# Performance work log

Measured on AMD Instinct MI355X. Metric: run time of the kernel, lower is better.

Reference implementation:

```python
import jax, jax.numpy as jnp
import numpy as np

IN_FEATURES = 4096
OUT_FEATURES = 4096
TOKENS = 8192
DENSITY = 0.5


def setup_inputs() -> dict:
    key = jax.random.key(0)
    kx, kw, km, kb = jax.random.split(key, 4)
    X = jax.random.normal(kx, (TOKENS, IN_FEATURES), dtype=jnp.float32)
    # kaiming-uniform-like init for weight [out, in]
    bound_w = np.sqrt(6.0 / IN_FEATURES) / np.sqrt(1.0 + 5.0)
    W = jax.random.uniform(kw, (OUT_FEATURES, IN_FEATURES), dtype=jnp.float32,
                           minval=-bound_w, maxval=bound_w)
    mask = jax.random.bernoulli(km, DENSITY, (OUT_FEATURES, IN_FEATURES))
    bound_b = 1.0 / np.sqrt(IN_FEATURES)
    b = jax.random.uniform(kb, (OUT_FEATURES,), dtype=jnp.float32,
                           minval=-bound_b, maxval=bound_b)
    return {"X": X, "W": W, "mask": mask, "b": b}


def reference(X, W, mask, b):
    # F.linear with a fixed-mask sparse weight: y = X @ (W * mask)^T + b
    Wm = W * mask.astype(W.dtype)  # masked weight [out, in]
    return jnp.einsum('ti,oi->to', X, Wm) + b
```

## Files before the change

### kernel.cpp

```cpp
#include <hip/hip_runtime.h>
#include <hip/hip_bf16.h>
#include <cstdint>
#include <cstddef>

#define M_TOK 8192
#define K_IN  4096
#define N_OUT 4096
#define NKS   384

typedef __attribute__((ext_vector_type(8))) short short8;
typedef __attribute__((ext_vector_type(4))) unsigned short ushort4v;
typedef __attribute__((ext_vector_type(4))) float f32x4;

__device__ inline void split_bf16(float x, unsigned short& h, unsigned short& l) {
    unsigned int u = __float_as_uint(x);
    unsigned int hb = (u + 0x7FFFu + ((u >> 16) & 1u)) >> 16;
    h = (unsigned short)hb;
    float hf = __uint_as_float(hb << 16);
    float r = x - hf;
    unsigned int ur = __float_as_uint(r);
    unsigned int lb = (ur + 0x7FFFu + ((ur >> 16) & 1u)) >> 16;
    l = (unsigned short)lb;
}

__global__ __launch_bounds__(256) void sl_cvt_x(const float* __restrict__ X,
                                                unsigned short* __restrict__ hi,
                                                unsigned short* __restrict__ lo, int n4) {
    int stride = gridDim.x * blockDim.x;
    for (int g = blockIdx.x * blockDim.x + threadIdx.x; g < n4; g += stride) {
        float4 v = ((const float4*)X)[g];
        float f[4] = {v.x, v.y, v.z, v.w};
        ushort4v h, l;
#pragma unroll
        for (int i = 0; i < 4; ++i) {
            unsigned short hh, ll;
            split_bf16(f[i], hh, ll);
            h[i] = hh; l[i] = ll;
        }
        ((ushort4v*)hi)[g] = h;
        ((ushort4v*)lo)[g] = l;
    }
}

__global__ __launch_bounds__(256) void sl_cvt_w(const float* __restrict__ W,
                                                const int* __restrict__ mask,
                                                unsigned short* __restrict__ hi,
                                                unsigned short* __restrict__ lo, int n4) {
    int stride = gridDim.x * blockDim.x;
    for (int g = blockIdx.x * blockDim.x + threadIdx.x; g < n4; g += stride) {
        float4 v = ((const float4*)W)[g];
        int4  mm = ((const int4*)mask)[g];
        float f[4];
        f[0] = mm.x ? v.x : 0.f;  f[1] = mm.y ? v.y : 0.f;
        f[2] = mm.z ? v.z : 0.f;  f[3] = mm.w ? v.w : 0.f;
        ushort4v h, l;
#pragma unroll
        for (int i = 0; i < 4; ++i) {
            unsigned short hh, ll;
            split_bf16(f[i], hh, ll);
            h[i] = hh; l[i] = ll;
        }
        ((ushort4v*)hi)[g] = h;
        ((ushort4v*)lo)[g] = l;
    }
}

__device__ inline void gload16(const void* g, void* l) {
    __builtin_amdgcn_global_load_lds(
        (const __attribute__((address_space(1))) void*)g,
        (__attribute__((address_space(3))) void*)l, 16, 0, 0);
}

__global__ __launch_bounds__(512, 2)
void sl_gemm_bf16x3(const unsigned short* __restrict__ Xhi,
                    const unsigned short* __restrict__ Xlo,
                    const unsigned short* __restrict__ Whi,
                    const unsigned short* __restrict__ Wlo,
                    const float* __restrict__ bias,
                    float* __restrict__ out) {
    __shared__ __align__(16) unsigned short As[4][256][32];
    __shared__ __align__(16) unsigned short Bs[4][256][32];

    const int bid = blockIdx.x;
    const int swz = (bid & 7) * 64 + (bid >> 3);
    const int bm = swz >> 4;
    const int bn = swz & 15;
    const int brow = bm * 256;
    const int bcol = bn * 256;

    const int tid = threadIdx.x;
    const int w   = tid >> 6;
    const int wm  = w >> 2, wn = w & 3;
    const int l   = tid & 63;
    const int r   = l & 15;
    const int kg  = l >> 4;

    const int swzCol = (((tid & 3) ^ ((tid >> 3) & 3)) * 8);
    const size_t aRow0 = (size_t)(brow + (tid >> 2)) * K_IN + swzCol;
    const size_t aRow1 = aRow0 + (size_t)128 * K_IN;
    const size_t bRow0 = (size_t)(bcol + (tid >> 2)) * K_IN + swzCol;
    const size_t bRow1 = bRow0 + (size_t)128 * K_IN;

    char* AsB = (char*)&As[0][0][0];
    char* BsB = (char*)&Bs[0][0][0];
    const int woff = w * 1024;

    const unsigned short* AsE = &As[0][0][0];
    const unsigned short* BsE = &Bs[0][0][0];
    const int slotOff = (kg ^ ((r >> 1) & 3)) * 8;
    const int aBaseE = (wm * 128 + r) * 32 + slotOff;
    const int bBaseE = (wn * 64 + r) * 32 + slotOff;

    f32x4 acc[8][4];
#pragma unroll
    for (int m = 0; m < 8; ++m)
#pragma unroll
        for (int n = 0; n < 4; ++n)
            acc[m][n] = (f32x4){0.f, 0.f, 0.f, 0.f};

#define STAGE_A(s_) do {                                                   \
    const int seg_ = (s_) >> 7;                                            \
    const unsigned short* pA_ = (seg_ == 1) ? Xlo : Xhi;                   \
    const size_t k_ = (size_t)((s_) & 127) * 32;                           \
    char* d_ = AsB + ((s_) & 3) * 16384 + woff;                            \
    gload16(pA_ + aRow0 + k_, d_);                                         \
    gload16(pA_ + aRow1 + k_, d_ + 8192);                                  \
} while (0)

#define STAGE_B(s_) do {                                                   \
    const int seg_ = (s_) >> 7;                                            \
    const unsigned short* pB_ = (seg_ == 2) ? Wlo : Whi;                   \
    const size_t k_ = (size_t)((s_) & 127) * 32;                           \
    char* d_ = BsB + ((s_) & 3) * 16384 + woff;                            \
    gload16(pB_ + bRow0 + k_, d_);                                         \
    gload16(pB_ + bRow1 + k_, d_ + 8192);                                  \
} while (0)

    STAGE_A(0); STAGE_B(0);
    STAGE_A(1); STAGE_B(1);
    STAGE_A(2); STAGE_B(2);

    for (int s = 0; s < NKS; ++s) {
        asm volatile("s_waitcnt vmcnt(8)" ::: "memory");
        __builtin_amdgcn_s_barrier();
        __builtin_amdgcn_sched_barrier(0);

        const int buf = (s & 3) * 8192;
        const bool st = (s + 3) < NKS;
        if (st) STAGE_A(s + 3);

        short8 a[4], b[4];
#pragma unroll
        for (int n = 0; n < 4; ++n)
            b[n] = *(const short8*)(BsE + buf + bBaseE + n * 512);
#pragma unroll
        for (int m = 0; m < 4; ++m)
            a[m] = *(const short8*)(AsE + buf + aBaseE + m * 512);

        __builtin_amdgcn_s_setprio(1);
#pragma unroll
        for (int m = 0; m < 4; ++m)
#pragma unroll
            for (int n = 0; n < 4; ++n)
                acc[m][n] = __builtin_amdgcn_mfma_f32_16x16x32_bf16(a[m], b[n], acc[m][n], 0, 0, 0);
        __builtin_amdgcn_s_setprio(0);

        if (st) STAGE_B(s + 3);
#pragma unroll
        for (int m = 0; m < 4; ++m)
            a[m] = *(const short8*)(AsE + buf + aBaseE + (m + 4) * 512);

        __builtin_amdgcn_s_setprio(1);
#pragma unroll
        for (int m = 0; m < 4; ++m)
#pragma unroll
            for (int n = 0; n < 4; ++n)
                acc[m + 4][n] = __builtin_amdgcn_mfma_f32_16x16x32_bf16(a[m], b[n], acc[m + 4][n], 0, 0, 0);
        __builtin_amdgcn_s_setprio(0);
    }
#undef STAGE_A
#undef STAGE_B

    float bv[4];
#pragma unroll
    for (int n = 0; n < 4; ++n)
        bv[n] = bias[bcol + wn * 64 + n * 16 + r];
    const int colBase = bcol + wn * 64 + r;
#pragma unroll
    for (int m = 0; m < 8; ++m) {
        const size_t rowb = (size_t)(brow + wm * 128 + m * 16 + kg * 4);
#pragma unroll
        for (int n = 0; n < 4; ++n) {
            const size_t c = (size_t)(colBase + n * 16);
#pragma unroll
            for (int q = 0; q < 4; ++q)
                out[(rowb + q) * N_OUT + c] = acc[m][n][q] + bv[n];
        }
    }
}

__global__ void sl_naive(const float* __restrict__ X, const float* __restrict__ W,
                         const int* __restrict__ mask, const float* __restrict__ bias,
                         float* __restrict__ out) {
    int o = blockIdx.x * blockDim.x + threadIdx.x;
    int t = blockIdx.y;
    if (o >= N_OUT) return;
    const float* xr = X + (size_t)t * K_IN;
    const float* wr = W + (size_t)o * K_IN;
    const int*   mr = mask + (size_t)o * K_IN;
    float s = 0.f;
    for (int k = 0; k < K_IN; ++k)
        s += xr[k] * (mr[k] ? wr[k] : 0.f);
    out[(size_t)t * N_OUT + o] = s + bias[o];
}

extern "C" void kernel_launch(void* const* d_in, const int* in_sizes, int n_in,
                              void* d_out, int out_size, void* d_ws, size_t ws_size,
                              hipStream_t stream) {
    (void)in_sizes; (void)n_in; (void)out_size;
    const float* X    = (const float*)d_in[0];
    const float* W    = (const float*)d_in[1];
    const int*   mask = (const int*)d_in[2];
    const float* bias = (const float*)d_in[3];
    float* out = (float*)d_out;

    const size_t xplane = (size_t)M_TOK * K_IN;
    const size_t wplane = (size_t)N_OUT * K_IN;
    const size_t need = (2 * xplane + 2 * wplane) * sizeof(unsigned short);

    if (ws_size < need) {
        dim3 g((N_OUT + 255) / 256, M_TOK);
        sl_naive<<<g, 256, 0, stream>>>(X, W, mask, bias, out);
        return;
    }

    unsigned short* Xhi = (unsigned short*)d_ws;
    unsigned short* Xlo = Xhi + xplane;
    unsigned short* Whi = Xlo + xplane;
    unsigned short* Wlo = Whi + wplane;

    sl_cvt_x<<<2048, 256, 0, stream>>>(X, Xhi, Xlo, (int)(xplane / 4));
    sl_cvt_w<<<2048, 256, 0, stream>>>(W, mask, Whi, Wlo, (int)(wplane / 4));
    sl_gemm_bf16x3<<<512, 512, 0, stream>>>(Xhi, Xlo, Whi, Wlo, bias, out);
}
```

Baseline: 1.139 ms.

## Fuse X/W conversion kernels and restructure GEMM loop into barrier-synced ping-pong phases

Merges the two bf16 hi/lo split kernels into a single launch that handles X and W on separate block ranges, with 8 elements per thread. In the GEMM main loop, the LDS fragment loads for each half are issued before the global-to-LDS prefetch, and the waits now sit inside each iteration at four block-wide barriers around the two MFMA clusters. The aim is to save one launch and to interleave memory and MFMA phases across waves. The extra barriers per k-step can add synchronization stalls if waves fail to overlap as intended.

```diff
diff --git a/kernel.cpp b/kernel.cpp
--- a/kernel.cpp
+++ b/kernel.cpp
@@ -9,7 +9,7 @@
 #define NKS   384
 
 typedef __attribute__((ext_vector_type(8))) short short8;
-typedef __attribute__((ext_vector_type(4))) unsigned short ushort4v;
+typedef __attribute__((ext_vector_type(8))) unsigned short ushort8;
 typedef __attribute__((ext_vector_type(4))) float f32x4;
 
 __device__ inline void split_bf16(float x, unsigned short& h, unsigned short& l) {
@@ -23,45 +23,54 @@
     l = (unsigned short)lb;
 }
 
-__global__ __launch_bounds__(256) void sl_cvt_x(const float* __restrict__ X,
-                                                unsigned short* __restrict__ hi,
-                                                unsigned short* __restrict__ lo, int n4) {
-    int stride = gridDim.x * blockDim.x;
-    for (int g = blockIdx.x * blockDim.x + threadIdx.x; g < n4; g += stride) {
-        float4 v = ((const float4*)X)[g];
-        float f[4] = {v.x, v.y, v.z, v.w};
-        ushort4v h, l;
-#pragma unroll
-        for (int i = 0; i < 4; ++i) {
-            unsigned short hh, ll;
-            split_bf16(f[i], hh, ll);
-            h[i] = hh; l[i] = ll;
-        }
-        ((ushort4v*)hi)[g] = h;
-        ((ushort4v*)lo)[g] = l;
-    }
-}
-
-__global__ __launch_bounds__(256) void sl_cvt_w(const float* __restrict__ W,
-                                                const int* __restrict__ mask,
-                                                unsigned short* __restrict__ hi,
-                                                unsigned short* __restrict__ lo, int n4) {
-    int stride = gridDim.x * blockDim.x;
-    for (int g = blockIdx.x * blockDim.x + threadIdx.x; g < n4; g += stride) {
-        float4 v = ((const float4*)W)[g];
-        int4  mm = ((const int4*)mask)[g];
-        float f[4];
-        f[0] = mm.x ? v.x : 0.f;  f[1] = mm.y ? v.y : 0.f;
-        f[2] = mm.z ? v.z : 0.f;  f[3] = mm.w ? v.w : 0.f;
-        ushort4v h, l;
-#pragma unroll
-        for (int i = 0; i < 4; ++i) {
-            unsigned short hh, ll;
-            split_bf16(f[i], hh, ll);
-            h[i] = hh; l[i] = ll;
-        }
-        ((ushort4v*)hi)[g] = h;
-        ((ushort4v*)lo)[g] = l;
+__global__ __launch_bounds__(256) void sl_cvt_fused(const float* __restrict__ X,
+                                                    const float* __restrict__ W,
+                                                    const int* __restrict__ mask,
+                                                    unsigned short* __restrict__ Xhi,
+                                                    unsigned short* __restrict__ Xlo,
+                                                    unsigned short* __restrict__ Whi,
+                                                    unsigned short* __restrict__ Wlo) {
+    const int b = blockIdx.x;
+    if (b < 2048) {
+        const int n8 = (M_TOK * K_IN) / 8;
+        const int stride = 2048 * 256;
+        for (int g = b * 256 + threadIdx.x; g < n8; g += stride) {
+            float4 v0 = ((const float4*)X)[(size_t)g * 2];
+            float4 v1 = ((const float4*)X)[(size_t)g * 2 + 1];
+            float f[8] = {v0.x, v0.y, v0.z, v0.w, v1.x, v1.y, v1.z, v1.w};
+            ushort8 h, l;
+#pragma unroll
+            for (int i = 0; i < 8; ++i) {
+                unsigned short hh, ll;
+                split_bf16(f[i], hh, ll);
+                h[i] = hh; l[i] = ll;
+            }
+            *(ushort8*)(Xhi + (size_t)g * 8) = h;
+            *(ushort8*)(Xlo + (size_t)g * 8) = l;
+        }
+    } else {
+        const int n8 = (N_OUT * K_IN) / 8;
+        const int stride = 2048 * 256;
+        for (int g = (b - 2048) * 256 + threadIdx.x; g < n8; g += stride) {
+            float4 v0 = ((const float4*)W)[(size_t)g * 2];
+            float4 v1 = ((const float4*)W)[(size_t)g * 2 + 1];
+            int4 m0 = ((const int4*)mask)[(size_t)g * 2];
+            int4 m1 = ((const int4*)mask)[(size_t)g * 2 + 1];
+            float f[8];
+            f[0] = m0.x ? v0.x : 0.f;  f[1] = m0.y ? v0.y : 0.f;
+            f[2] = m0.z ? v0.z : 0.f;  f[3] = m0.w ? v0.w : 0.f;
+            f[4] = m1.x ? v1.x : 0.f;  f[5] = m1.y ? v1.y : 0.f;
+            f[6] = m1.z ? v1.z : 0.f;  f[7] = m1.w ? v1.w : 0.f;
+            ushort8 h, l;
+#pragma unroll
+            for (int i = 0; i < 8; ++i) {
+                unsigned short hh, ll;
+                split_bf16(f[i], hh, ll);
+                h[i] = hh; l[i] = ll;
+            }
+            *(ushort8*)(Whi + (size_t)g * 8) = h;
+            *(ushort8*)(Wlo + (size_t)g * 8) = l;
+        }
     }
 }
 
@@ -139,44 +148,82 @@
     STAGE_A(0); STAGE_B(0);
     STAGE_A(1); STAGE_B(1);
     STAGE_A(2); STAGE_B(2);
+    asm volatile("s_waitcnt vmcnt(8)" ::: "memory");
+    __builtin_amdgcn_s_barrier();
+    __builtin_amdgcn_sched_barrier(0);
 
     for (int s = 0; s < NKS; ++s) {
-        asm volatile("s_waitcnt vmcnt(8)" ::: "memory");
-        __builtin_amdgcn_s_barrier();
-        __builtin_amdgcn_sched_barrier(0);
-
         const int buf = (s & 3) * 8192;
         const bool st = (s + 3) < NKS;
+
+        short8 b0 = *(const short8*)(BsE + buf + bBaseE);
+        short8 b1 = *(const short8*)(BsE + buf + bBaseE + 512);
+        short8 b2 = *(const short8*)(BsE + buf + bBaseE + 1024);
+        short8 b3 = *(const short8*)(BsE + buf + bBaseE + 1536);
+        short8 p0 = *(const short8*)(AsE + buf + aBaseE);
+        short8 p1 = *(const short8*)(AsE + buf + aBaseE + 512);
+        short8 p2 = *(const short8*)(AsE + buf + aBaseE + 1024);
+        short8 p3 = *(const short8*)(AsE + buf + aBaseE + 1536);
         if (st) STAGE_A(s + 3);
 
-        short8 a[4], b[4];
-#pragma unroll
-        for (int n = 0; n < 4; ++n)
-            b[n] = *(const short8*)(BsE + buf + bBaseE + n * 512);
-#pragma unroll
-        for (int m = 0; m < 4; ++m)
-            a[m] = *(const short8*)(AsE + buf + aBaseE + m * 512);
-
+        __builtin_amdgcn_s_barrier();
+        asm volatile("s_waitcnt lgkmcnt(0)" ::: "memory");
+        __builtin_amdgcn_sched_barrier(0);
         __builtin_amdgcn_s_setprio(1);
-#pragma unroll
-        for (int m = 0; m < 4; ++m)
-#pragma unroll
-            for (int n = 0; n < 4; ++n)
-                acc[m][n] = __builtin_amdgcn_mfma_f32_16x16x32_bf16(a[m], b[n], acc[m][n], 0, 0, 0);
+        acc[0][0] = __builtin_amdgcn_mfma_f32_16x16x32_bf16(p0, b0, acc[0][0], 0, 0, 0);
+        acc[0][1] = __builtin_amdgcn_mfma_f32_16x16x32_bf16(p0, b1, acc[0][1], 0, 0, 0);
+        acc[0][2] = __builtin_amdgcn_mfma_f32_16x16x32_bf16(p0, b2, acc[0][2], 0, 0, 0);
+        acc[0][3] = __builtin_amdgcn_mfma_f32_16x16x32_bf16(p0, b3, acc[0][3], 0, 0, 0);
+        acc[1][0] = __builtin_amdgcn_mfma_f32_16x16x32_bf16(p1, b0, acc[1][0], 0, 0, 0);
+        acc[1][1] = __builtin_amdgcn_mfma_f32_16x16x32_bf16(p1, b1, acc[1][1], 0, 0, 0);
+        acc[1][2] = __builtin_amdgcn_mfma_f32_16x16x32_bf16(p1, b2, acc[1][2], 0, 0, 0);
+        acc[1][3] = __builtin_amdgcn_mfma_f32_16x16x32_bf16(p1, b3, acc[1][3], 0, 0, 0);
+        acc[2][0] = __builtin_amdgcn_mfma_f32_16x16x32_bf16(p2, b0, acc[2][0], 0, 0, 0);
+        acc[2][1] = __builtin_amdgcn_mfma_f32_16x16x32_bf16(p2, b1, acc[2][1], 0, 0, 0);
+        acc[2][2] = __builtin_amdgcn_mfma_f32_16x16x32_bf16(p2, b2, acc[2][2], 0, 0, 0);
+        acc[2][3] = __builtin_amdgcn_mfma_f32_16x16x32_bf16(p2, b3, acc[2][3], 0, 0, 0);
+        acc[3][0] = __builtin_amdgcn_mfma_f32_16x16x32_bf16(p3, b0, acc[3][0], 0, 0, 0);
+        acc[3][1] = __builtin_amdgcn_mfma_f32_16x16x32_bf16(p3, b1, acc[3][1], 0, 0, 0);
+        acc[3][2] = __builtin_amdgcn_mfma_f32_16x16x32_bf16(p3, b2, acc[3][2], 0, 0, 0);
+        acc[3][3] = __builtin_amdgcn_mfma_f32_16x16x32_bf16(p3, b3, acc[3][3], 0, 0, 0);
         __builtin_amdgcn_s_setprio(0);
-
-        if (st) STAGE_B(s + 3);
-#pragma unroll
-        for (int m = 0; m < 4; ++m)
-            a[m] = *(const short8*)(AsE + buf + aBaseE + (m + 4) * 512);
-
+        __builtin_amdgcn_s_barrier();
+        __builtin_amdgcn_sched_barrier(0);
+
+        short8 q0 = *(const short8*)(AsE + buf + aBaseE + 2048);
+        short8 q1 = *(const short8*)(AsE + buf + aBaseE + 2560);
+        short8 q2 = *(const short8*)(AsE + buf + aBaseE + 3072);
+        short8 q3 = *(const short8*)(AsE + buf + aBaseE + 3584);
+        if (st) {
+            STAGE_B(s + 3);
+            asm volatile("s_waitcnt vmcnt(8)" ::: "memory");
+        } else {
+            asm volatile("s_waitcnt vmcnt(0)" ::: "memory");
+        }
+
+        __builtin_amdgcn_s_barrier();
+        asm volatile("s_waitcnt lgkmcnt(0)" ::: "memory");
+        __builtin_amdgcn_sched_barrier(0);
         __builtin_amdgcn_s_setprio(1);
-#pragma unroll
-        for (int m = 0; m < 4; ++m)
-#pragma unroll
-            for (int n = 0; n < 4; ++n)
-                acc[m + 4][n] = __builtin_amdgcn_mfma_f32_16x16x32_bf16(a[m], b[n], acc[m + 4][n], 0, 0, 0);
+        acc[4][0] = __builtin_amdgcn_mfma_f32_16x16x32_bf16(q0, b0, acc[4][0], 0, 0, 0);
+        acc[4][1] = __builtin_amdgcn_mfma_f32_16x16x32_bf16(q0, b1, acc[4][1], 0, 0, 0);
+        acc[4][2] = __builtin_amdgcn_mfma_f32_16x16x32_bf16(q0, b2, acc[4][2], 0, 0, 0);
+        acc[4][3] = __builtin_amdgcn_mfma_f32_16x16x32_bf16(q0, b3, acc[4][3], 0, 0, 0);
+        acc[5][0] = __builtin_amdgcn_mfma_f32_16x16x32_bf16(q1, b0, acc[5][0], 0, 0, 0);
+        acc[5][1] = __builtin_amdgcn_mfma_f32_16x16x32_bf16(q1, b1, acc[5][1], 0, 0, 0);
+        acc[5][2] = __builtin_amdgcn_mfma_f32_16x16x32_bf16(q1, b2, acc[5][2], 0, 0, 0);
+        acc[5][3] = __builtin_amdgcn_mfma_f32_16x16x32_bf16(q1, b3, acc[5][3], 0, 0, 0);
+        acc[6][0] = __builtin_amdgcn_mfma_f32_16x16x32_bf16(q2, b0, acc[6][0], 0, 0, 0);
+        acc[6][1] = __builtin_amdgcn_mfma_f32_16x16x32_bf16(q2, b1, acc[6][1], 0, 0, 0);
+        acc[6][2] = __builtin_amdgcn_mfma_f32_16x16x32_bf16(q2, b2, acc[6][2], 0, 0, 0);
+        acc[6][3] = __builtin_amdgcn_mfma_f32_16x16x32_bf16(q2, b3, acc[6][3], 0, 0, 0);
+        acc[7][0] = __builtin_amdgcn_mfma_f32_16x16x32_bf16(q3, b0, acc[7][0], 0, 0, 0);
+        acc[7][1] = __builtin_amdgcn_mfma_f32_16x16x32_bf16(q3, b1, acc[7][1], 0, 0, 0);
+        acc[7][2] = __builtin_amdgcn_mfma_f32_16x16x32_bf16(q3, b2, acc[7][2], 0, 0, 0);
+        acc[7][3] = __builtin_amdgcn_mfma_f32_16x16x32_bf16(q3, b3, acc[7][3], 0, 0, 0);
         __builtin_amdgcn_s_setprio(0);
+        __builtin_amdgcn_s_barrier();
+        __builtin_amdgcn_sched_barrier(0);
     }
 #undef STAGE_A
 #undef STAGE_B
@@ -239,7 +286,6 @@
     unsigned short* Whi = Xlo + xplane;
     unsigned short* Wlo = Whi + wplane;
 
-    sl_cvt_x<<<2048, 256, 0, stream>>>(X, Xhi, Xlo, (int)(xplane / 4));
-    sl_cvt_w<<<2048, 256, 0, stream>>>(W, mask, Whi, Wlo, (int)(wplane / 4));
+    sl_cvt_fused<<<4096, 256, 0, stream>>>(X, W, mask, Xhi, Xlo, Whi, Wlo);
     sl_gemm_bf16x3<<<512, 512, 0, stream>>>(Xhi, Xlo, Whi, Wlo, bias, out);
 }
```

Measured after the change: 1.111 ms. 2.4% less time.
